# Performance work log

Measured on AMD Instinct MI355X. Metric: run time of the kernel, lower is better.

The kernel has to match this reference:

```python
import jax, jax.numpy as jnp
import numpy as np
from jax import lax

N, T, IN = 64, 1024, 64
H = 512
H2 = H // 2   # 256
H4 = H // 4   # 128
H10 = H // 10 # 51


def _lstm(x, Wih, Whh, bih, bhh):
    """PyTorch-style LSTM, batch_first. x: [N,T,in]. Returns hs [N,T,h], h_T, c_T."""
    n, t, _ = x.shape
    h = Whh.shape[1]
    b = bih + bhh

    def step(carry, xt):
        hprev, cprev = carry
        gates = xt @ Wih.T + hprev @ Whh.T + b
        i, f, g, o = jnp.split(gates, 4, axis=-1)
        i = jax.nn.sigmoid(i)
        f = jax.nn.sigmoid(f)
        g = jnp.tanh(g)
        o = jax.nn.sigmoid(o)
        c = f * cprev + i * g
        hnew = o * jnp.tanh(c)
        return (hnew, c), hnew

    h0 = jnp.zeros((n, h), x.dtype)
    c0 = jnp.zeros((n, h), x.dtype)
    (hT, cT), hs = lax.scan(step, (h0, c0), x.transpose(1, 0, 2))
    return hs.transpose(1, 0, 2), hT, cT


def _causal_self_attention(hs):
    """Unscaled dot-product causal attention, equivalent to the python loop."""
    n, t, h = hs.shape
    scores = jnp.einsum('nth,nsh->nts', hs, hs)  # [N,T,T]
    mask = jnp.tril(jnp.ones((t, t), bool))
    scores = jnp.where(mask[None], scores, -jnp.inf)
    attn = jax.nn.softmax(scores, axis=-1)
    return jnp.einsum('nts,nsh->nth', attn, hs)


def setup_inputs() -> dict:
    key = jax.random.key(0)
    ks = jax.random.split(key, 16)
    s = 0.05
    return {
        'x': jax.random.normal(ks[0], (N, T, IN), jnp.float32),
        'W_ih1': jax.random.normal(ks[1], (4 * H, IN), jnp.float32) * s,
        'W_hh1': jax.random.normal(ks[2], (4 * H, H), jnp.float32) * s,
        'b_ih1': jax.random.normal(ks[3], (4 * H,), jnp.float32) * s,
        'b_hh1': jax.random.normal(ks[4], (4 * H,), jnp.float32) * s,
        'W_ih2': jax.random.normal(ks[5], (4 * H2, H), jnp.float32) * s,
        'W_hh2': jax.random.normal(ks[6], (4 * H2, H2), jnp.float32) * s,
        'b_ih2': jax.random.normal(ks[7], (4 * H2,), jnp.float32) * s,
        'b_hh2': jax.random.normal(ks[8], (4 * H2,), jnp.float32) * s,
        'fc1_w': jax.random.normal(ks[9], (H4, 2 * H2), jnp.float32) * s,
        'fc1_b': jax.random.normal(ks[10], (H4,), jnp.float32) * s,
        'fc2_w': jax.random.normal(ks[11], (H10, H4), jnp.float32) * s,
        'fc2_b': jax.random.normal(ks[12], (H10,), jnp.float32) * s,
        'fc3_w': jax.random.normal(ks[13], (1, H10), jnp.float32) * s,
        'fc3_b': jax.random.normal(ks[14], (1,), jnp.float32) * s,
    }


def reference(x, W_ih1, W_hh1, b_ih1, b_hh1, W_ih2, W_hh2, b_ih2, b_hh2,
              fc1_w, fc1_b, fc2_w, fc2_b, fc3_w, fc3_b):
    out, h1, c1 = _lstm(x, W_ih1, W_hh1, b_ih1, b_hh1)     # [N,T,H]
    out, h2, c2 = _lstm(out, W_ih2, W_hh2, b_ih2, b_hh2)   # [N,T,H2]
    contexts = _causal_self_attention(out)                  # [N,T,H2]
    out = jnp.concatenate((contexts, out), axis=2)          # [N,T,2*H2]
    out = jax.nn.relu(out @ fc1_w.T + fc1_b)                # dropout_ratio=0 -> identity
    out = jax.nn.relu(out @ fc2_w.T + fc2_b)
    out = out @ fc3_w.T + fc3_b                              # [N,T,1]
    return out, h1, c1, h2, c2
```

## Files before the change

kernel.cpp:

```cpp
#include <hip/hip_runtime.h>
#include <hip/hip_bf16.h>

#define N_   64
#define T_   1024
#define IN_  64
#define H1_  512
#define H2_  256
#define NG   4
#define NU1  16
#define NU2  8
#define RING 8
#define RING2 4
#define SENT 0xAAAAAAAAu

typedef __bf16 bf16x8 __attribute__((ext_vector_type(8)));
typedef float  f32x4  __attribute__((ext_vector_type(4)));
typedef unsigned int u32x4 __attribute__((ext_vector_type(4)));
typedef unsigned short u16x8 __attribute__((ext_vector_type(8)));
typedef unsigned long long u64;
typedef __hip_bfloat16 bf16_t;

#define OFF_FLG2  8192u
#define OFF_QUE   12288u
#define ZERO_BYTES 16384u
#define OFF_H1R   16384u
#define OFF_H2R   540672u
#define OFF_XB    671744u
#define OFF_W1    9060352u
#define OFF_W2    11419648u
#define OFF_B1    12992512u
#define OFF_B2    13000704u
#define OFF_FC1W  13004800u
#define OFF_FC2W  13135872u
#define OFF_HS2   13152256u
#define OFF_BURN  46706688u

__device__ __forceinline__ bf16x8 ld16(const bf16_t* p) {
  u32x4 u = *reinterpret_cast<const u32x4*>(p);
  return __builtin_bit_cast(bf16x8, u);
}
__device__ __forceinline__ u64 ld64_mall(const void* p) {
  return __hip_atomic_load((const u64*)p, __ATOMIC_RELAXED, __HIP_MEMORY_SCOPE_AGENT);
}
__device__ __forceinline__ void st4_mall(bf16_t* p, unsigned v) {
  __hip_atomic_store((unsigned*)p, v, __ATOMIC_RELAXED, __HIP_MEMORY_SCOPE_AGENT);
}
__device__ __forceinline__ unsigned ldflag(unsigned* p) {
  return __hip_atomic_load(p, __ATOMIC_RELAXED, __HIP_MEMORY_SCOPE_AGENT);
}
__device__ __forceinline__ bool sentok(u64 w) {
  return ((unsigned)w != SENT) && ((unsigned)(w >> 32) != SENT);
}
__device__ __forceinline__ f32x4 mfma_bf16(bf16x8 a, bf16x8 b, f32x4 c) {
  return __builtin_amdgcn_mfma_f32_16x16x32_bf16(a, b, c, 0, 0, 0);
}
__device__ __forceinline__ float sigf(float x) { return 1.f / (1.f + __expf(-x)); }
__device__ __forceinline__ float tanh_fast(float x) {
  float e = __expf(-2.f * fabsf(x));
  float r = (1.f - e) / (1.f + e);
  return x < 0.f ? -r : r;
}
__device__ __forceinline__ unsigned short bf16_bits(float v) {
  __hip_bfloat16 b = __float2bfloat16(v);
  return *reinterpret_cast<unsigned short*>(&b);
}

__global__ void setup_kernel(const float* __restrict__ x,
    const float* __restrict__ Wih1, const float* __restrict__ Whh1,
    const float* __restrict__ bih1, const float* __restrict__ bhh1,
    const float* __restrict__ Wih2, const float* __restrict__ Whh2,
    const float* __restrict__ bih2, const float* __restrict__ bhh2,
    const float* __restrict__ fc1w, const float* __restrict__ fc2w,
    char* __restrict__ ws)
{
  bf16_t* xb = (bf16_t*)(ws + OFF_XB);
  bf16_t* w1 = (bf16_t*)(ws + OFF_W1);
  bf16_t* w2 = (bf16_t*)(ws + OFF_W2);
  float*  b1 = (float*)(ws + OFF_B1);
  float*  b2 = (float*)(ws + OFF_B2);
  bf16_t* f1 = (bf16_t*)(ws + OFF_FC1W);
  bf16_t* f2 = (bf16_t*)(ws + OFF_FC2W);
  const long E0 = 4194304, E1 = E0 + 1179648, E2 = E1 + 786432,
             E3 = E2 + 2048, E4 = E3 + 1024, E5 = E4 + 65536, E6 = E5 + 8192;
  for (long i = blockIdx.x * (long)blockDim.x + threadIdx.x; i < E6;
       i += (long)gridDim.x * blockDim.x) {
    if (i < E0) {
      xb[i] = __float2bfloat16(x[i]);
    } else if (i < E1) {
      long idx = i - E0; long j = idx / 576, k = idx % 576;
      float v = (k < 64) ? Wih1[j * 64 + k] : Whh1[j * 512 + (k - 64)];
      w1[idx] = __float2bfloat16(v);
    } else if (i < E2) {
      long idx = i - E1; long j = idx / 768, k = idx % 768;
      float v = (k < 512) ? Wih2[j * 512 + k] : Whh2[j * 256 + (k - 512)];
      w2[idx] = __float2bfloat16(v);
    } else if (i < E3) {
      long idx = i - E2; b1[idx] = bih1[idx] + bhh1[idx];
    } else if (i < E4) {
      long idx = i - E3; b2[idx] = bih2[idx] + bhh2[idx];
    } else if (i < E5) {
      long idx = i - E4; f1[idx] = __float2bfloat16(fc1w[idx]);
    } else {
      long idx = i - E5; long j = idx / 128, k = idx % 128;
      f2[idx] = __float2bfloat16(j < 51 ? fc2w[j * 128 + k] : 0.f);
    }
  }
}

__global__ __launch_bounds__(256, 1) void fused_kernel(char* __restrict__ ws,
    const float* __restrict__ fc1b, const float* __restrict__ fc2b,
    const float* __restrict__ fc3w, const float* __restrict__ fc3b,
    float* __restrict__ dout)
{
  const bf16_t* xb  = (const bf16_t*)(ws + OFF_XB);
  const bf16_t* W1  = (const bf16_t*)(ws + OFF_W1);
  const bf16_t* W2  = (const bf16_t*)(ws + OFF_W2);
  const float*  b1  = (const float*)(ws + OFF_B1);
  const float*  b2  = (const float*)(ws + OFF_B2);
  bf16_t* h1r = (bf16_t*)(ws + OFF_H1R);
  bf16_t* h2r = (bf16_t*)(ws + OFF_H2R);
  bf16_t* hs2 = (bf16_t*)(ws + OFF_HS2);
  unsigned* flag2 = (unsigned*)(ws + OFF_FLG2);

  __shared__ __align__(16) char smem[55296];

  const int tid  = threadIdx.x;
  const int wave = tid >> 6;
  const int lane = tid & 63;
  const int l15  = lane & 15;
  const int quad = lane >> 4;
  const int bx   = blockIdx.x;
  const f32x4 z = {0.f, 0.f, 0.f, 0.f};

  if (bx < NG * NU1) {
    const int g = bx >> 4, u = bx & 15, u0 = u * 32;
    bf16_t* hstage = (bf16_t*)smem;
    float*  gbuf   = (float*)(smem + 18688);
    bf16x8 wf[18][2];
    #pragma unroll
    for (int i = 0; i < 18; ++i)
      #pragma unroll
      for (int nt = 0; nt < 2; ++nt)
        wf[i][nt] = ld16(W1 + (size_t)(wave * H1_ + u0 + nt * 16 + l15) * 576 + i * 32 + quad * 8);

    const int sr = tid >> 4;
    const int myp = tid & 15;
    const int row = tid >> 4, ui = (tid & 15) * 2;
    const int nrow = g * 16 + row;
    unsigned* bp = flag2 + (g * NU2 + (tid & 7)) * 32;
    float bi[2], bff[2], bg[2], bo[2], creg[2];
    #pragma unroll
    for (int j = 0; j < 2; ++j) {
      int ug = u0 + ui + j;
      bi[j]  = b1[ug];         bff[j] = b1[H1_ + ug];
      bg[j]  = b1[2*H1_ + ug]; bo[j]  = b1[3*H1_ + ug];
      creg[j] = 0.f;
    }
    #pragma unroll
    for (int s = 0; s < RING; ++s)
      st4_mall(h1r + ((size_t)(g * RING + s) * 16 + row) * 512 + u0 + ui, SENT);

    unsigned fpre = 0;
    #pragma unroll 1
    for (int t = 0; t < T_; ++t) {
      u64 xv = *(const u64*)(xb + ((size_t)(g*16 + sr) * T_ + t) * IN_ + myp * 4);
      if (t >= 7 && (int)fpre < t - 6) {
        while ((int)ldflag(bp) < t - 6) __builtin_amdgcn_s_sleep(1);
      }
      fpre = ldflag(bp);
      if (t == 0) {
        #pragma unroll
        for (int k = 0; k < 8; ++k)
          *(u64*)(hstage + sr * 584 + 64 + myp * 32 + k * 4) = 0ull;
      } else {
        const u64* src = (const u64*)(h1r + ((size_t)(g * RING + ((t-1) & 7)) * 16 + sr) * 512 + myp * 32);
        u64 w[8];
        for (;;) {
          #pragma unroll
          for (int k = 0; k < 8; ++k) w[k] = ld64_mall(src + k);
          bool ok = true;
          #pragma unroll
          for (int k = 0; k < 8; ++k) ok &= sentok(w[k]);
          if (ok) break;
        }
        #pragma unroll
        for (int k = 0; k < 8; ++k)
          *(u64*)(hstage + sr * 584 + 64 + myp * 32 + k * 4) = w[k];
      }
      *(u64*)(hstage + sr * 584 + myp * 4) = xv;
      __syncthreads();
      st4_mall(h1r + ((size_t)(g * RING + ((t+1) & 7)) * 16 + row) * 512 + u0 + ui, SENT);
      f32x4 acc[2] = {z, z}, acd[2] = {z, z};
      #pragma unroll
      for (int ki = 0; ki < 9; ++ki) {
        bf16x8 aw = ld16(hstage + l15 * 584 + ki * 32 + quad * 8);
        acc[0] = mfma_bf16(aw, wf[ki][0], acc[0]);
        acc[1] = mfma_bf16(aw, wf[ki][1], acc[1]);
      }
      #pragma unroll
      for (int ki = 9; ki < 18; ++ki) {
        bf16x8 aw = ld16(hstage + l15 * 584 + ki * 32 + quad * 8);
        acd[0] = mfma_bf16(aw, wf[ki][0], acd[0]);
        acd[1] = mfma_bf16(aw, wf[ki][1], acd[1]);
      }
      acc[0] += acd[0]; acc[1] += acd[1];
      #pragma unroll
      for (int nt = 0; nt < 2; ++nt)
        #pragma unroll
        for (int r = 0; r < 4; ++r)
          gbuf[(wave * 16 + quad * 4 + r) * 33 + nt * 16 + l15] = acc[nt][r];
      __syncthreads();
      {
        unsigned pack = 0;
        float hv[2];
        #pragma unroll
        for (int j = 0; j < 2; ++j) {
          int col = ui + j;
          float iv = sigf(gbuf[(0*16 + row) * 33 + col] + bi[j]);
          float fv = sigf(gbuf[(1*16 + row) * 33 + col] + bff[j]);
          float gv = tanh_fast(gbuf[(2*16 + row) * 33 + col] + bg[j]);
          float ov = sigf(gbuf[(3*16 + row) * 33 + col] + bo[j]);
          float c = fv * creg[j] + iv * gv;
          creg[j] = c;
          float h = ov * tanh_fast(c);
          hv[j] = h;
          pack |= (unsigned)bf16_bits(h) << (16 * j);
        }
        st4_mall(h1r + ((size_t)(g * RING + (t & 7)) * 16 + row) * 512 + u0 + ui, pack);
        if (t == T_ - 1) {
          #pragma unroll
          for (int j = 0; j < 2; ++j) {
            dout[65536 + nrow * H1_ + u0 + ui + j] = hv[j];
            dout[98304 + nrow * H1_ + u0 + ui + j] = creg[j];
          }
        }
      }
    }
  } else if (bx < NG * NU1 + NG * NU2) {
    const int b2x = bx - NG * NU1;
    const int g = b2x >> 3, u = b2x & 7, u0 = u * 32;
    bf16_t* hstage = (bf16_t*)smem;
    float*  gbuf   = (float*)(smem + 25088);
    bf16x8 wf[24][2];
    #pragma unroll
    for (int i = 0; i < 24; ++i)
      #pragma unroll
      for (int nt = 0; nt < 2; ++nt)
        wf[i][nt] = ld16(W2 + (size_t)(wave * H2_ + u0 + nt * 16 + l15) * 768 + i * 32 + quad * 8);

    const int sr = tid >> 4;
    const int q  = tid & 15;
    const int row = tid >> 4, ui = (tid & 15) * 2;
    const int nrow = g * 16 + row;
    unsigned* myflag = flag2 + (g * NU2 + u) * 32;
    float bi[2], bff[2], bg[2], bo[2], creg[2];
    #pragma unroll
    for (int j = 0; j < 2; ++j) {
      int ug = u0 + ui + j;
      bi[j]  = b2[ug];         bff[j] = b2[H2_ + ug];
      bg[j]  = b2[2*H2_ + ug]; bo[j]  = b2[3*H2_ + ug];
      creg[j] = 0.f;
    }
    #pragma unroll
    for (int s = 0; s < RING2; ++s)
      st4_mall(h2r + ((size_t)(g * RING2 + s) * 16 + row) * 256 + u0 + ui, SENT);

    u64 pf[8];
    #pragma unroll 1
    for (int t = 0; t < T_; ++t) {
      {
        const u64* s1 = (const u64*)(h1r + ((size_t)(g * RING + (t & 7)) * 16 + sr) * 512 + q * 32);
        bool good = (t > 0);
        if (good) {
          #pragma unroll
          for (int k = 0; k < 8; ++k) good &= sentok(pf[k]);
        }
        if (!good) {
          for (;;) {
            #pragma unroll
            for (int k = 0; k < 8; ++k) pf[k] = ld64_mall(s1 + k);
            bool ok = true;
            #pragma unroll
            for (int k = 0; k < 8; ++k) ok &= sentok(pf[k]);
            if (ok) break;
          }
        }
        #pragma unroll
        for (int k = 0; k < 8; ++k)
          *(u64*)(hstage + sr * 784 + q * 32 + k * 4) = pf[k];
      }
      if (t == 0) {
        #pragma unroll
        for (int k = 0; k < 4; ++k)
          *(u64*)(hstage + sr * 784 + 512 + q * 16 + k * 4) = 0ull;
      } else {
        const u64* s2 = (const u64*)(h2r + ((size_t)(g * RING2 + ((t-1) & 3)) * 16 + sr) * 256 + q * 16);
        u64 w[4];
        for (;;) {
          #pragma unroll
          for (int k = 0; k < 4; ++k) w[k] = ld64_mall(s2 + k);
          bool ok = true;
          #pragma unroll
          for (int k = 0; k < 4; ++k) ok &= sentok(w[k]);
          if (ok) break;
        }
        #pragma unroll
        for (int k = 0; k < 4; ++k)
          *(u64*)(hstage + sr * 784 + 512 + q * 16 + k * 4) = w[k];
      }
      __syncthreads();
      if (tid == 0 && t > 0)
        __hip_atomic_store(myflag, (unsigned)t, __ATOMIC_RELAXED, __HIP_MEMORY_SCOPE_AGENT);
      st4_mall(h2r + ((size_t)(g * RING2 + ((t+1) & 3)) * 16 + row) * 256 + u0 + ui, SENT);
      f32x4 acc[2] = {z, z}, acd[2] = {z, z};
      #pragma unroll
      for (int ki = 0; ki < 12; ++ki) {
        bf16x8 aw = ld16(hstage + l15 * 784 + ki * 32 + quad * 8);
        acc[0] = mfma_bf16(aw, wf[ki][0], acc[0]);
        acc[1] = mfma_bf16(aw, wf[ki][1], acc[1]);
      }
      #pragma unroll
      for (int ki = 12; ki < 24; ++ki) {
        bf16x8 aw = ld16(hstage + l15 * 784 + ki * 32 + quad * 8);
        acd[0] = mfma_bf16(aw, wf[ki][0], acd[0]);
        acd[1] = mfma_bf16(aw, wf[ki][1], acd[1]);
      }
      acc[0] += acd[0]; acc[1] += acd[1];
      #pragma unroll
      for (int nt = 0; nt < 2; ++nt)
        #pragma unroll
        for (int r = 0; r < 4; ++r)
          gbuf[(wave * 16 + quad * 4 + r) * 33 + nt * 16 + l15] = acc[nt][r];
      __syncthreads();
      {
        unsigned pack = 0;
        float hv[2];
        #pragma unroll
        for (int j = 0; j < 2; ++j) {
          int col = ui + j;
          float iv = sigf(gbuf[(0*16 + row) * 33 + col] + bi[j]);
          float fv = sigf(gbuf[(1*16 + row) * 33 + col] + bff[j]);
          float gv = tanh_fast(gbuf[(2*16 + row) * 33 + col] + bg[j]);
          float ov = sigf(gbuf[(3*16 + row) * 33 + col] + bo[j]);
          float c = fv * creg[j] + iv * gv;
          creg[j] = c;
          float h = ov * tanh_fast(c);
          hv[j] = h;
          pack |= (unsigned)bf16_bits(h) << (16 * j);
        }
        st4_mall(h2r + ((size_t)(g * RING2 + (t & 3)) * 16 + row) * 256 + u0 + ui, pack);
        st4_mall(hs2 + ((size_t)nrow * T_ + t) * H2_ + u0 + ui, pack);
        if (t == T_ - 1) {
          #pragma unroll
          for (int j = 0; j < 2; ++j) {
            dout[131072 + nrow * H2_ + u0 + ui + j] = hv[j];
            dout[147456 + nrow * H2_ + u0 + ui + j] = creg[j];
          }
        }
      }
      if (t + 1 < T_) {
        const u64* nx = (const u64*)(h1r + ((size_t)(g * RING + ((t+1) & 7)) * 16 + sr) * 512 + q * 32);
        #pragma unroll
        for (int k = 0; k < 8; ++k) pf[k] = ld64_mall(nx + k);
      }
    }
    __syncthreads();
    if (tid == 0)
      __hip_atomic_store(myflag, (unsigned)T_, __ATOMIC_RELAXED, __HIP_MEMORY_SCOPE_AGENT);
  }

  __syncthreads();
  {
    const bf16_t* f1w = (const bf16_t*)(ws + OFF_FC1W);
    const bf16_t* f2w = (const bf16_t*)(ws + OFF_FC2W);
    unsigned* queue = (unsigned*)(ws + OFF_QUE);
    unsigned short* vtile = (unsigned short*)smem;
    bf16_t* plds   = (bf16_t*)(smem + 36864);
    bf16_t* ctxlds = (bf16_t*)smem;
    bf16_t* act1   = (bf16_t*)(smem + 36864);
    float*  act2   = (float*)smem;
    volatile int* itemslot = (volatile int*)(smem + 55040);
    float burn = 1.0f;

    for (;;) {
      if (tid == 0) *itemslot = (int)atomicAdd(queue, 1u);
      __syncthreads();
      const int item = *itemslot;
      __syncthreads();
      if (item >= 1024) break;
      const int qt = item >> 6, n = item & 63, q0 = qt * 64, gg = n >> 4;

      {
        const int need = q0 + 64;
        if (tid < 64) {
          unsigned* p = (lane < NU2) ? flag2 + (gg * NU2 + lane) * 32 : nullptr;
          bool ok = (p == nullptr) || ((int)ldflag(p) >= need);
          while (!__all(ok)) {
            #pragma unroll
            for (int k = 0; k < 32; ++k) burn = fmaf(burn, 1.0000001f, 1e-7f);
            __builtin_amdgcn_s_sleep(4);
            ok = (p == nullptr) || ((int)ldflag(p) >= need);
          }
        }
        __syncthreads();
      }

      bf16x8 aq[8];
      #pragma unroll
      for (int ks = 0; ks < 8; ++ks)
        aq[ks] = ld16(hs2 + ((size_t)n * T_ + q0 + wave * 16 + l15) * H2_ + ks * 32 + quad * 8);
      f32x4 o[16];
      #pragma unroll
      for (int ct = 0; ct < 16; ++ct) o[ct] = z;
      float m_run[4], l_run[4];
      #pragma unroll
      for (int r = 0; r < 4; ++r) { m_run[r] = -1e30f; l_run[r] = 0.f; }
      bf16_t* pw = plds + wave * 1152;

      #pragma unroll 1
      for (int st = 0; st <= qt; ++st) {
        const int s0 = st * 64;
        __syncthreads();
        #pragma unroll
        for (int it = 0; it < 8; ++it) {
          int s  = (tid >> 3) + (it & 1) * 32;
          int c0 = (tid & 7) * 8 + (it >> 1) * 64;
          u16x8 v = *reinterpret_cast<const u16x8*>(
              (const unsigned short*)hs2 + ((size_t)n * T_ + s0 + s) * H2_ + c0);
          #pragma unroll
          for (int j = 0; j < 8; ++j) {
            int ch = c0 + j;
            int sw = (s & 7) | ((((s >> 3) ^ (ch >> 3)) & 7) << 3);
            vtile[ch * 72 + sw] = v[j];
          }
        }
        __syncthreads();
        f32x4 sc[4] = {z, z, z, z};
        #pragma unroll
        for (int ks = 0; ks < 8; ++ks) {
          #pragma unroll
          for (int nt = 0; nt < 4; ++nt) {
            bf16x8 bk = ld16(hs2 + ((size_t)n * T_ + s0 + nt * 16 + l15) * H2_ + ks * 32 + quad * 8);
            sc[nt] = mfma_bf16(aq[ks], bk, sc[nt]);
          }
        }
        if (st == qt) {
          int qg = q0 + wave * 16 + quad * 4;
          #pragma unroll
          for (int nt = 0; nt < 4; ++nt) {
            int sg = s0 + nt * 16 + l15;
            #pragma unroll
            for (int r = 0; r < 4; ++r)
              if (sg > qg + r) sc[nt][r] = -1e30f;
          }
        }
        float alpha[4];
        #pragma unroll
        for (int r = 0; r < 4; ++r) {
          float tm = fmaxf(fmaxf(sc[0][r], sc[1][r]), fmaxf(sc[2][r], sc[3][r]));
          tm = fmaxf(tm, __shfl_xor(tm, 1, 16));
          tm = fmaxf(tm, __shfl_xor(tm, 2, 16));
          tm = fmaxf(tm, __shfl_xor(tm, 4, 16));
          tm = fmaxf(tm, __shfl_xor(tm, 8, 16));
          float mnew = fmaxf(m_run[r], tm);
          alpha[r] = __expf(m_run[r] - mnew);
          m_run[r] = mnew;
          float ts = 0.f;
          #pragma unroll
          for (int nt = 0; nt < 4; ++nt) {
            float p = __expf(sc[nt][r] - mnew);
            sc[nt][r] = p;
            ts += p;
          }
          ts += __shfl_xor(ts, 1, 16);
          ts += __shfl_xor(ts, 2, 16);
          ts += __shfl_xor(ts, 4, 16);
          ts += __shfl_xor(ts, 8, 16);
          l_run[r] = l_run[r] * alpha[r] + ts;
        }
        #pragma unroll
        for (int ct = 0; ct < 16; ++ct)
          #pragma unroll
          for (int r = 0; r < 4; ++r)
            o[ct][r] *= alpha[r];
        #pragma unroll
        for (int nt = 0; nt < 4; ++nt)
          #pragma unroll
          for (int r = 0; r < 4; ++r)
            pw[(quad * 4 + r) * 72 + nt * 16 + l15] = __float2bfloat16(sc[nt][r]);
        #pragma unroll
        for (int ks2 = 0; ks2 < 2; ++ks2) {
          bf16x8 ap = ld16(pw + l15 * 72 + ks2 * 32 + quad * 8);
          #pragma unroll
          for (int ct = 0; ct < 16; ++ct) {
            int ch = ct * 16 + l15;
            int blk = ((ks2 * 4 + quad) ^ (ch >> 3)) & 7;
            bf16x8 bv = ld16((bf16_t*)vtile + ch * 72 + blk * 8);
            o[ct] = mfma_bf16(ap, bv, o[ct]);
          }
        }
      }
      __syncthreads();
      float inv[4];
      #pragma unroll
      for (int r = 0; r < 4; ++r) inv[r] = 1.f / l_run[r];
      #pragma unroll
      for (int ct = 0; ct < 16; ++ct)
        #pragma unroll
        for (int r = 0; r < 4; ++r)
          ctxlds[(wave * 16 + quad * 4 + r) * 264 + ct * 16 + l15] =
              __float2bfloat16(o[ct][r] * inv[r]);
      __syncthreads();

      f32x4 a1[4][2];
      #pragma unroll
      for (int mt = 0; mt < 4; ++mt) { a1[mt][0] = z; a1[mt][1] = z; }
      #pragma unroll
      for (int ks = 0; ks < 16; ++ks) {
        bf16x8 af[4];
        if (ks < 8) {
          #pragma unroll
          for (int mt = 0; mt < 4; ++mt)
            af[mt] = ld16(ctxlds + (mt * 16 + l15) * 264 + ks * 32 + quad * 8);
        } else {
          #pragma unroll
          for (int mt = 0; mt < 4; ++mt)
            af[mt] = ld16(hs2 + ((size_t)n * T_ + q0 + mt * 16 + l15) * H2_ + (ks - 8) * 32 + quad * 8);
        }
        #pragma unroll
        for (int nt = 0; nt < 2; ++nt) {
          bf16x8 bw = ld16(f1w + (size_t)(wave * 32 + nt * 16 + l15) * 512 + ks * 32 + quad * 8);
          #pragma unroll
          for (int mt = 0; mt < 4; ++mt)
            a1[mt][nt] = mfma_bf16(af[mt], bw, a1[mt][nt]);
        }
      }
      #pragma unroll
      for (int mt = 0; mt < 4; ++mt)
        #pragma unroll
        for (int nt = 0; nt < 2; ++nt)
          #pragma unroll
          for (int r = 0; r < 4; ++r) {
            int ch = wave * 32 + nt * 16 + l15;
            float v = a1[mt][nt][r] + fc1b[ch];
            act1[(mt * 16 + quad * 4 + r) * 136 + ch] = __float2bfloat16(fmaxf(v, 0.f));
          }
      __syncthreads();

      f32x4 a2[4] = {z, z, z, z};
      #pragma unroll
      for (int ks = 0; ks < 4; ++ks) {
        bf16x8 bw = ld16(f2w + (wave * 16 + l15) * 128 + ks * 32 + quad * 8);
        #pragma unroll
        for (int mt = 0; mt < 4; ++mt) {
          bf16x8 af = ld16(act1 + (mt * 16 + l15) * 136 + ks * 32 + quad * 8);
          a2[mt] = mfma_bf16(af, bw, a2[mt]);
        }
      }
      __syncthreads();
      #pragma unroll
      for (int mt = 0; mt < 4; ++mt)
        #pragma unroll
        for (int r = 0; r < 4; ++r) {
          int ch = wave * 16 + l15;
          int rw = mt * 16 + quad * 4 + r;
          float v = a2[mt][r] + (ch < 51 ? fc2b[ch] : 0.f);
          act2[rw * 68 + ch] = fmaxf(v, 0.f);
        }
      __syncthreads();
      if (tid < 64) {
        float s = fc3b[0];
        for (int c = 0; c < 51; ++c) s += act2[tid * 68 + c] * fc3w[c];
        dout[(size_t)n * T_ + q0 + tid] = s;
      }
      __syncthreads();
    }
    if (burn == 0.1234567f)
      ((float*)(ws + OFF_BURN))[tid] = burn;
  }
}

extern "C" void kernel_launch(void* const* d_in, const int* in_sizes, int n_in,
                              void* d_out, int out_size, void* d_ws, size_t ws_size,
                              hipStream_t stream) {
  (void)in_sizes; (void)n_in; (void)out_size; (void)ws_size;
  const float* x    = (const float*)d_in[0];
  const float* Wih1 = (const float*)d_in[1];
  const float* Whh1 = (const float*)d_in[2];
  const float* bih1 = (const float*)d_in[3];
  const float* bhh1 = (const float*)d_in[4];
  const float* Wih2 = (const float*)d_in[5];
  const float* Whh2 = (const float*)d_in[6];
  const float* bih2 = (const float*)d_in[7];
  const float* bhh2 = (const float*)d_in[8];
  const float* fc1w = (const float*)d_in[9];
  const float* fc1b = (const float*)d_in[10];
  const float* fc2w = (const float*)d_in[11];
  const float* fc2b = (const float*)d_in[12];
  const float* fc3w = (const float*)d_in[13];
  const float* fc3b = (const float*)d_in[14];
  char* ws  = (char*)d_ws;
  float* out = (float*)d_out;

  hipMemsetAsync(ws, 0, ZERO_BYTES, stream);
  setup_kernel<<<2048, 256, 0, stream>>>(x, Wih1, Whh1, bih1, bhh1,
                                         Wih2, Whh2, bih2, bhh2, fc1w, fc2w, ws);
  fused_kernel<<<256, 256, 0, stream>>>(ws, fc1b, fc2b, fc3w, fc3b, out);
}
```

Measured before the change: 3.145 ms.

## Interleave two batch groups per LSTM block to halve recurrent block count

```diff
diff --git a/kernel.cpp b/kernel.cpp
--- a/kernel.cpp
+++ b/kernel.cpp
@@ -122,7 +122,7 @@
   bf16_t* hs2 = (bf16_t*)(ws + OFF_HS2);
   unsigned* flag2 = (unsigned*)(ws + OFF_FLG2);
 
-  __shared__ __align__(16) char smem[55296];
+  __shared__ __align__(16) char smem[67072];
 
   const int tid  = threadIdx.x;
   const int wave = tid >> 6;
@@ -132,10 +132,13 @@
   const int bx   = blockIdx.x;
   const f32x4 z = {0.f, 0.f, 0.f, 0.f};
 
-  if (bx < NG * NU1) {
-    const int g = bx >> 4, u = bx & 15, u0 = u * 32;
-    bf16_t* hstage = (bf16_t*)smem;
-    float*  gbuf   = (float*)(smem + 18688);
+  if (bx < 32) {
+    const int p = bx >> 4, u = bx & 15, u0 = u * 32;
+    const int gA = p * 2, gB = p * 2 + 1;
+    bf16_t* hstA = (bf16_t*)smem;
+    bf16_t* hstB = (bf16_t*)(smem + 18688);
+    float*  gbA  = (float*)(smem + 37376);
+    float*  gbB  = (float*)(smem + 45824);
     bf16x8 wf[18][2];
     #pragma unroll
     for (int i = 0; i < 18; ++i)
@@ -146,23 +149,25 @@
     const int sr = tid >> 4;
     const int myp = tid & 15;
     const int row = tid >> 4, ui = (tid & 15) * 2;
-    const int nrow = g * 16 + row;
-    unsigned* bp = flag2 + (g * NU2 + (tid & 7)) * 32;
-    float bi[2], bff[2], bg[2], bo[2], creg[2];
+    unsigned* bpA = flag2 + (gA * NU2 + (tid & 7)) * 32;
+    unsigned* bpB = flag2 + (gB * NU2 + (tid & 7)) * 32;
+    float bi[2], bff[2], bg[2], bo[2];
+    float cregA[2] = {0.f, 0.f}, cregB[2] = {0.f, 0.f};
     #pragma unroll
     for (int j = 0; j < 2; ++j) {
       int ug = u0 + ui + j;
       bi[j]  = b1[ug];         bff[j] = b1[H1_ + ug];
       bg[j]  = b1[2*H1_ + ug]; bo[j]  = b1[3*H1_ + ug];
-      creg[j] = 0.f;
     }
     #pragma unroll
-    for (int s = 0; s < RING; ++s)
-      st4_mall(h1r + ((size_t)(g * RING + s) * 16 + row) * 512 + u0 + ui, SENT);
-
-    unsigned fpre = 0;
-    #pragma unroll 1
-    for (int t = 0; t < T_; ++t) {
+    for (int s = 0; s < RING; ++s) {
+      st4_mall(h1r + ((size_t)(gA * RING + s) * 16 + row) * 512 + u0 + ui, SENT);
+      st4_mall(h1r + ((size_t)(gB * RING + s) * 16 + row) * 512 + u0 + ui, SENT);
+    }
+    unsigned fpA = 0, fpB = 0;
+
+    auto l1half = [&](int g, bf16_t* hstage, float* gbuf, float (&creg)[2],
+                      unsigned& fpre, unsigned* bp, int t) {
       u64 xv = *(const u64*)(xb + ((size_t)(g*16 + sr) * T_ + t) * IN_ + myp * 4);
       if (t >= 7 && (int)fpre < t - 6) {
         while ((int)ldflag(bp) < t - 6) __builtin_amdgcn_s_sleep(1);
@@ -228,6 +233,7 @@
         }
         st4_mall(h1r + ((size_t)(g * RING + (t & 7)) * 16 + row) * 512 + u0 + ui, pack);
         if (t == T_ - 1) {
+          int nrow = g * 16 + row;
           #pragma unroll
           for (int j = 0; j < 2; ++j) {
             dout[65536 + nrow * H1_ + u0 + ui + j] = hv[j];
@@ -235,12 +241,21 @@
           }
         }
       }
-    }
-  } else if (bx < NG * NU1 + NG * NU2) {
-    const int b2x = bx - NG * NU1;
-    const int g = b2x >> 3, u = b2x & 7, u0 = u * 32;
-    bf16_t* hstage = (bf16_t*)smem;
-    float*  gbuf   = (float*)(smem + 25088);
+    };
+
+    #pragma unroll 1
+    for (int t = 0; t < T_; ++t) {
+      l1half(gA, hstA, gbA, cregA, fpA, bpA, t);
+      l1half(gB, hstB, gbB, cregB, fpB, bpB, t);
+    }
+  } else if (bx < 48) {
+    const int b2x = bx - 32;
+    const int p = b2x >> 3, u = b2x & 7, u0 = u * 32;
+    const int gA = p * 2, gB = p * 2 + 1;
+    bf16_t* hstA = (bf16_t*)smem;
+    bf16_t* hstB = (bf16_t*)(smem + 25088);
+    float*  gbA  = (float*)(smem + 50176);
+    float*  gbB  = (float*)(smem + 58624);
     bf16x8 wf[24][2];
     #pragma unroll
     for (int i = 0; i < 24; ++i)
@@ -251,23 +266,25 @@
     const int sr = tid >> 4;
     const int q  = tid & 15;
     const int row = tid >> 4, ui = (tid & 15) * 2;
-    const int nrow = g * 16 + row;
-    unsigned* myflag = flag2 + (g * NU2 + u) * 32;
-    float bi[2], bff[2], bg[2], bo[2], creg[2];
+    unsigned* flA = flag2 + (gA * NU2 + u) * 32;
+    unsigned* flB = flag2 + (gB * NU2 + u) * 32;
+    float bi[2], bff[2], bg[2], bo[2];
+    float cregA[2] = {0.f, 0.f}, cregB[2] = {0.f, 0.f};
     #pragma unroll
     for (int j = 0; j < 2; ++j) {
       int ug = u0 + ui + j;
       bi[j]  = b2[ug];         bff[j] = b2[H2_ + ug];
       bg[j]  = b2[2*H2_ + ug]; bo[j]  = b2[3*H2_ + ug];
-      creg[j] = 0.f;
     }
     #pragma unroll
-    for (int s = 0; s < RING2; ++s)
-      st4_mall(h2r + ((size_t)(g * RING2 + s) * 16 + row) * 256 + u0 + ui, SENT);
-
-    u64 pf[8];
-    #pragma unroll 1
-    for (int t = 0; t < T_; ++t) {
+    for (int s = 0; s < RING2; ++s) {
+      st4_mall(h2r + ((size_t)(gA * RING2 + s) * 16 + row) * 256 + u0 + ui, SENT);
+      st4_mall(h2r + ((size_t)(gB * RING2 + s) * 16 + row) * 256 + u0 + ui, SENT);
+    }
+    u64 pfA[8], pfB[8];
+
+    auto l2half = [&](int g, bf16_t* hstage, float* gbuf, float (&creg)[2],
+                      u64 (&pf)[8], unsigned* myflag, int t) {
       {
         const u64* s1 = (const u64*)(h1r + ((size_t)(g * RING + (t & 7)) * 16 + sr) * 512 + q * 32);
         bool good = (t > 0);
@@ -348,6 +365,7 @@
           hv[j] = h;
           pack |= (unsigned)bf16_bits(h) << (16 * j);
         }
+        int nrow = g * 16 + row;
         st4_mall(h2r + ((size_t)(g * RING2 + (t & 3)) * 16 + row) * 256 + u0 + ui, pack);
         st4_mall(hs2 + ((size_t)nrow * T_ + t) * H2_ + u0 + ui, pack);
         if (t == T_ - 1) {
@@ -363,10 +381,18 @@
         #pragma unroll
         for (int k = 0; k < 8; ++k) pf[k] = ld64_mall(nx + k);
       }
+    };
+
+    #pragma unroll 1
+    for (int t = 0; t < T_; ++t) {
+      l2half(gA, hstA, gbA, cregA, pfA, flA, t);
+      l2half(gB, hstB, gbB, cregB, pfB, flB, t);
     }
     __syncthreads();
-    if (tid == 0)
-      __hip_atomic_store(myflag, (unsigned)T_, __ATOMIC_RELAXED, __HIP_MEMORY_SCOPE_AGENT);
+    if (tid == 0) {
+      __hip_atomic_store(flA, (unsigned)T_, __ATOMIC_RELAXED, __HIP_MEMORY_SCOPE_AGENT);
+      __hip_atomic_store(flB, (unsigned)T_, __ATOMIC_RELAXED, __HIP_MEMORY_SCOPE_AGENT);
+    }
   }
 
   __syncthreads();
```

Measured after the change: 5.579 ms. 1.77x slower.
